# Performance work log

Hardware: AMD Instinct MI355X
Metric: run time of the kernel (lower is better)

The kernel has to match this reference:

```python
import jax, jax.numpy as jnp
import numpy as np

DOT_TEMP = 0.05  # hardcoded in the original forward (self.temperature is never used)
EPS = 1e-6


def setup_inputs() -> dict:
    key = jax.random.key(0)
    k1, k2 = jax.random.split(key)
    bsz, n_views, dim = 4096, 2, 128
    features = jax.random.normal(k1, (bsz, n_views, dim), dtype=jnp.float32)
    labels = jax.random.randint(k2, (bsz,), 0, 100, dtype=jnp.int32)
    return {"features": features, "labels": labels}


def reference(features, labels):
    bsz, V, dim = features.shape  # V = n_views; contrast_mode='all' -> anchor_count = contrast_count = V
    n = V * bsz

    # contrast_feature = cat(unbind(features, dim=1), dim=0): [view0 batch; view1 batch; ...]
    cf = jnp.transpose(features, (1, 0, 2)).reshape(n, dim)  # [n, dim]

    # positive mask: eq(labels, labels.T) tiled, diagonal zeroed
    eq = labels[:, None] == labels[None, :]  # [bsz, bsz]
    mask = jnp.tile(eq.astype(jnp.float32), (V, V))  # [n, n]
    mask = mask * (1.0 - jnp.eye(n, dtype=jnp.float32))

    # Key simplification (exactly faithful): mask3[i] (eq) and mask2[i] (ne) are complementary,
    # so unique(cat(where(mask3[i]), where(mask2[i]))) == arange(n) for every row. Hence each
    # loop iteration in the original computes the SAME scalar from the full gram matrix.
    lab2 = jnp.tile(labels, V)  # matches labels2[:n] layout in the original
    diff = (lab2[:, None] != lab2[None, :]).astype(jnp.float32)  # [n, n]

    dots = jnp.matmul(cf, cf.T) / DOT_TEMP  # [n, n]
    dm = dots * diff
    maxd = jnp.max(dm, axis=1, keepdims=True)
    S = jnp.sum(jnp.exp(dm - maxd))  # exp_terms.sum() -- identical for every valid row
    N = jnp.sum(diff)                # different_label_mask.sum()

    # rows with mask2[i].sum() == 0 are skipped (left at zero)
    valid = jnp.tile(jnp.any(labels[None, :] != labels[:, None], axis=1), V)  # [n]
    xv = jnp.where(valid, S, 0.0)
    nv = jnp.where(valid, N, 0.0)

    # if not all(negtivesum == 0): x = x / negtivesum   (safe divide for skipped rows)
    all_zero = jnp.all(nv == 0.0)
    xv = jnp.where(all_zero, xv, xv / jnp.where(nv == 0.0, 1.0, nv))

    log_prob = -jnp.log(xv[:, None] + EPS)  # [n, 1], broadcast over columns
    msum = jnp.sum(mask, axis=1)
    msum_safe = jnp.where(msum == 0.0, 1.0, msum)
    pos_logits = -jnp.sum(mask * log_prob, axis=1) / msum_safe  # [n]
    loss = jnp.mean(pos_logits)  # mean over view(anchor_count, bsz) == overall mean
    return loss
```

## Files before the change

kernel.cpp:

```cpp
#include <hip/hip_runtime.h>
#include <hip/hip_bf16.h>
#include <stdint.h>

#define N_TOT 8192
#define BSZ   4096
#define NCH   32
#define SQS   5.3715827f

typedef _Float16 f16x8 __attribute__((ext_vector_type(8)));
typedef float f32x4 __attribute__((ext_vector_type(4)));

__device__ __forceinline__ float fast_exp2(float x) {
#if __has_builtin(__builtin_amdgcn_exp2f)
  return __builtin_amdgcn_exp2f(x);
#else
  return exp2f(x);
#endif
}
#define EXP2(x) fast_exp2(x)

__global__ __launch_bounds__(256) void prep14_kernel(
    const float* __restrict__ feat, const int* __restrict__ labels,
    _Float16* __restrict__ H2, unsigned char* __restrict__ lab8, int* __restrict__ cnt) {
  if (blockIdx.x == 512) {
    __shared__ int h[128];
    if (threadIdx.x < 128) h[threadIdx.x] = 0;
    __syncthreads();
    for (int i = threadIdx.x; i < BSZ; i += 256) atomicAdd(&h[labels[i] & 127], 1);
    __syncthreads();
    if (threadIdx.x < 128) cnt[threadIdx.x] = h[threadIdx.x];
    for (int i = threadIdx.x; i < N_TOT; i += 256)
      lab8[i] = (unsigned char)labels[i & (BSZ - 1)];
    return;
  }
  int idx = blockIdx.x * 256 + threadIdx.x;
  int rowblk = idx >> 8, inner = idx & 255;
  int k8 = inner >> 4, rlo = inner & 15;
  int r = rowblk * 16 + rlo;
  int b = r & (BSZ - 1), v = r >> 12;
  const float* src = feat + ((size_t)((b << 1) + v) << 7) + k8 * 8;
  float4 x0 = *(const float4*)src;
  float4 x1 = *(const float4*)(src + 4);
  float xs[8] = {x0.x, x0.y, x0.z, x0.w, x1.x, x1.y, x1.z, x1.w};
  f16x8 hv;
#pragma unroll
  for (int jj = 0; jj < 8; ++jj) hv[jj] = (_Float16)(xs[jj] * SQS);
  *(f16x8*)((char*)H2 + (size_t)idx * 16) = hv;
}

__global__ __launch_bounds__(256) void gemm14_kernel(
    const _Float16* __restrict__ H2, const int* __restrict__ labels,
    const unsigned char* __restrict__ lab8,
    float* __restrict__ pM, float* __restrict__ pS) {
  __shared__ __align__(16) char ldsB[2][16384];

  int orig = blockIdx.x;
  int xcd = orig & 7, j = orig >> 3;
  int cg = xcd * 4 + (j & 3);
  int rg = j >> 2;
  int wave = threadIdx.x >> 6, lane = threadIdx.x & 63;
  int lq = lane >> 4, lr16 = lane & 15;

  const uint32_t rowbase = (uint32_t)rg * 128 + wave * 32;
  const char* Hb = (const char*)H2;
  const uint32_t laneoff = lq * 256 + lr16 * 16;

  int lrw[2];
#pragma unroll
  for (int m = 0; m < 2; ++m)
    lrw[m] = labels[(rowbase + m * 16 + lr16) & (BSZ - 1)];

  f16x8 Areg[2][4];
#pragma unroll
  for (int m = 0; m < 2; ++m)
#pragma unroll
    for (int kb = 0; kb < 4; ++kb)
      Areg[m][kb] = *(const f16x8*)(Hb + (size_t)((rowbase >> 4) + m) * 4096 + kb * 1024 + laneoff);

  const char* Bsrc = Hb + (size_t)cg * 65536;

#define STAGE(T, BUF)                                                                     \
  {                                                                                       \
    _Pragma("unroll")                                                                     \
    for (int i = 0; i < 4; ++i) {                                                         \
      int chunk = wave * 4 + i;                                                           \
      __builtin_amdgcn_global_load_lds(                                                   \
          (const __attribute__((address_space(1))) void*)(Bsrc + ((T) * 4 + (chunk >> 2)) * 4096 + (chunk & 3) * 1024 + lane * 16), \
          (__attribute__((address_space(3))) void*)(&ldsB[BUF][chunk * 1024]), 16, 0, 0); \
    }                                                                                     \
  }

  STAGE(0, 0);
  asm volatile("s_waitcnt vmcnt(0)" ::: "memory");
  __builtin_amdgcn_sched_barrier(0);
  __builtin_amdgcn_s_barrier();

  f32x4 acc[2][4];
  float mxv[2] = {-3.0e38f, -3.0e38f}, sv[2] = {0.0f, 0.0f};

#pragma unroll
  for (int t = 0; t < 4; ++t) {
    if (t < 3) STAGE(t + 1, (t + 1) & 1);
    const char* Bb = ldsB[t & 1];

#pragma unroll
    for (int m = 0; m < 2; ++m)
#pragma unroll
      for (int ni = 0; ni < 4; ++ni) acc[m][ni] = f32x4{0.f, 0.f, 0.f, 0.f};

    f16x8 Bf[2][4];
#pragma unroll
    for (int ni = 0; ni < 4; ++ni)
      Bf[0][ni] = *(const f16x8*)(Bb + ni * 4096 + laneoff);
#pragma unroll
    for (int kb = 0; kb < 4; ++kb) {
      int cur = kb & 1;
      if (kb < 3) {
#pragma unroll
        for (int ni = 0; ni < 4; ++ni)
          Bf[cur ^ 1][ni] = *(const f16x8*)(Bb + ni * 4096 + (kb + 1) * 1024 + laneoff);
      }
      __builtin_amdgcn_s_setprio(1);
#pragma unroll
      for (int m = 0; m < 2; ++m)
#pragma unroll
        for (int ni = 0; ni < 4; ++ni)
          acc[m][ni] = __builtin_amdgcn_mfma_f32_16x16x32_f16(Bf[cur][ni], Areg[m][kb], acc[m][ni], 0, 0, 0);
      __builtin_amdgcn_s_setprio(0);
    }

    uint32_t labw[4];
#pragma unroll
    for (int ni = 0; ni < 4; ++ni)
      labw[ni] = *(const uint32_t*)(lab8 + cg * 256 + t * 64 + ni * 16 + lq * 4);
    int lc[16];
#pragma unroll
    for (int i = 0; i < 16; ++i) lc[i] = (labw[i >> 2] >> (8 * (i & 3))) & 255;

#pragma unroll
    for (int m = 0; m < 2; ++m) {
      float v[16];
#pragma unroll
      for (int ni = 0; ni < 4; ++ni)
#pragma unroll
        for (int r = 0; r < 4; ++r)
          v[ni * 4 + r] = (lrw[m] != lc[ni * 4 + r]) ? acc[m][ni][r] : 0.0f;
      float m01 = fmaxf(v[0], v[1]),  m23 = fmaxf(v[2], v[3]);
      float m45 = fmaxf(v[4], v[5]),  m67 = fmaxf(v[6], v[7]);
      float m89 = fmaxf(v[8], v[9]),  mab = fmaxf(v[10], v[11]);
      float mcd = fmaxf(v[12], v[13]), mef = fmaxf(v[14], v[15]);
      float bm = fmaxf(fmaxf(fmaxf(m01, m23), fmaxf(m45, m67)),
                       fmaxf(fmaxf(m89, mab), fmaxf(mcd, mef)));
      float nm = fmaxf(mxv[m], bm);
      float s0 = 0.f, s1 = 0.f, s2 = 0.f, s3 = 0.f;
#pragma unroll
      for (int r = 0; r < 4; ++r) {
        s0 += EXP2(v[r] - nm);
        s1 += EXP2(v[4 + r] - nm);
        s2 += EXP2(v[8 + r] - nm);
        s3 += EXP2(v[12 + r] - nm);
      }
      sv[m] = sv[m] * EXP2(mxv[m] - nm) + ((s0 + s1) + (s2 + s3));
      mxv[m] = nm;
    }

    asm volatile("s_waitcnt vmcnt(0)" ::: "memory");
    __builtin_amdgcn_sched_barrier(0);
    __builtin_amdgcn_s_barrier();
  }
#undef STAGE

#pragma unroll
  for (int m = 0; m < 2; ++m) {
    float M = mxv[m], S = sv[m];
#pragma unroll
    for (int off = 16; off < 64; off <<= 1) {
      float Mo = __shfl_xor(M, off, 64);
      float So = __shfl_xor(S, off, 64);
      float Mn = fmaxf(M, Mo);
      S = S * EXP2(M - Mn) + So * EXP2(Mo - Mn);
      M = Mn;
    }
    if (lane < 16) {
      pM[(size_t)cg * N_TOT + rowbase + m * 16 + lane] = M;
      pS[(size_t)cg * N_TOT + rowbase + m * 16 + lane] = S;
    }
  }
}

__global__ __launch_bounds__(256) void rowred14_kernel(const float* __restrict__ pM,
                                                       const float* __restrict__ pS,
                                                       float* __restrict__ blockS) {
  int row = blockIdx.x * 256 + threadIdx.x;
  float M = -3.0e38f;
#pragma unroll
  for (int c = 0; c < NCH; ++c) M = fmaxf(M, pM[(size_t)c * N_TOT + row]);
  float s = 0.0f;
#pragma unroll
  for (int c = 0; c < NCH; ++c)
    s += pS[(size_t)c * N_TOT + row] * EXP2(pM[(size_t)c * N_TOT + row] - M);
  __shared__ float red[256];
  red[threadIdx.x] = s;
  __syncthreads();
  for (int st = 128; st > 0; st >>= 1) {
    if (threadIdx.x < st) red[threadIdx.x] += red[threadIdx.x + st];
    __syncthreads();
  }
  if (threadIdx.x == 0) blockS[blockIdx.x] = red[0];
}

__global__ void final14_kernel(const float* __restrict__ blockS, const int* __restrict__ cnt,
                               float* __restrict__ out) {
  int lane = threadIdx.x;
  float s = (lane < 32) ? blockS[lane] : 0.0f;
#pragma unroll
  for (int off = 1; off < 64; off <<= 1) s += __shfl_xor(s, off, 64);
  if (lane == 0) {
    double Stot = (double)s;
    long long sumsq = 0;
    int nval = 0;
    for (int c = 0; c < 128; ++c) {
      long long cc = cnt[c];
      sumsq += cc * cc;
      if (cc > 0 && cc < BSZ) nval += 2 * (int)cc;
    }
    double Nd = (double)N_TOT * (double)N_TOT - 4.0 * (double)sumsq;
    float loss;
    if (Nd <= 0.0 || nval == 0) {
      loss = logf(1e-6f);
    } else {
      float x = (float)(Stot / Nd);
      loss = ((float)nval * logf(x + 1e-6f) +
              (float)(N_TOT - nval) * logf(1e-6f)) / (float)N_TOT;
    }
    out[0] = loss;
  }
}

extern "C" void kernel_launch(void* const* d_in, const int* in_sizes, int n_in,
                              void* d_out, int out_size, void* d_ws, size_t ws_size,
                              hipStream_t stream) {
  const float* feat = (const float*)d_in[0];
  const int* labels = (const int*)d_in[1];
  float* out = (float*)d_out;

  char* ws = (char*)d_ws;
  _Float16* H2        = (_Float16*)(ws);
  unsigned char* lab8 = (unsigned char*)(ws + 2097152);
  float* pM           = (float*)(ws + 2105344);
  float* pS           = (float*)(ws + 3153920);
  int* cnt            = (int*)(ws + 4202496);
  float* blockS       = (float*)(ws + 4203008);

  prep14_kernel<<<513, 256, 0, stream>>>(feat, labels, H2, lab8, cnt);
  gemm14_kernel<<<2048, 256, 0, stream>>>(H2, labels, lab8, pM, pS);
  rowred14_kernel<<<32, 256, 0, stream>>>(pM, pS, blockS);
  final14_kernel<<<1, 64, 0, stream>>>(blockS, cnt, out);
}
```

Before: 46.07 us.

## Fuse final reduction into rowred via atomic counter and trim GEMM registers

Merges the single-block final kernel into the row-reduction kernel. The last block to finish, detected with an atomic counter that the prep kernel resets, computes the loss, which removes one kernel launch. The GEMM kernel gains a launch_bounds occupancy hint of 4 blocks and reads row labels from the byte label array. It also drops the B-fragment double buffering and masks the accumulators in place, cutting register use in exchange for less overlap between LDS loads and MFMA.

```diff
diff --git a/kernel.cpp b/kernel.cpp
--- a/kernel.cpp
+++ b/kernel.cpp
@@ -19,9 +19,10 @@
 }
 #define EXP2(x) fast_exp2(x)
 
-__global__ __launch_bounds__(256) void prep14_kernel(
+__global__ __launch_bounds__(256) void prep16_kernel(
     const float* __restrict__ feat, const int* __restrict__ labels,
-    _Float16* __restrict__ H2, unsigned char* __restrict__ lab8, int* __restrict__ cnt) {
+    _Float16* __restrict__ H2, unsigned char* __restrict__ lab8, int* __restrict__ cnt,
+    int* __restrict__ ctr) {
   if (blockIdx.x == 512) {
     __shared__ int h[128];
     if (threadIdx.x < 128) h[threadIdx.x] = 0;
@@ -29,6 +30,7 @@
     for (int i = threadIdx.x; i < BSZ; i += 256) atomicAdd(&h[labels[i] & 127], 1);
     __syncthreads();
     if (threadIdx.x < 128) cnt[threadIdx.x] = h[threadIdx.x];
+    if (threadIdx.x == 0) *ctr = 0;
     for (int i = threadIdx.x; i < N_TOT; i += 256)
       lab8[i] = (unsigned char)labels[i & (BSZ - 1)];
     return;
@@ -48,9 +50,8 @@
   *(f16x8*)((char*)H2 + (size_t)idx * 16) = hv;
 }
 
-__global__ __launch_bounds__(256) void gemm14_kernel(
-    const _Float16* __restrict__ H2, const int* __restrict__ labels,
-    const unsigned char* __restrict__ lab8,
+__global__ __launch_bounds__(256, 4) void gemm16_kernel(
+    const _Float16* __restrict__ H2, const unsigned char* __restrict__ lab8,
     float* __restrict__ pM, float* __restrict__ pS) {
   __shared__ __align__(16) char ldsB[2][16384];
 
@@ -68,7 +69,7 @@
   int lrw[2];
 #pragma unroll
   for (int m = 0; m < 2; ++m)
-    lrw[m] = labels[(rowbase + m * 16 + lr16) & (BSZ - 1)];
+    lrw[m] = lab8[rowbase + m * 16 + lr16];
 
   f16x8 Areg[2][4];
 #pragma unroll
@@ -108,24 +109,18 @@
 #pragma unroll
       for (int ni = 0; ni < 4; ++ni) acc[m][ni] = f32x4{0.f, 0.f, 0.f, 0.f};
 
-    f16x8 Bf[2][4];
-#pragma unroll
-    for (int ni = 0; ni < 4; ++ni)
-      Bf[0][ni] = *(const f16x8*)(Bb + ni * 4096 + laneoff);
 #pragma unroll
     for (int kb = 0; kb < 4; ++kb) {
-      int cur = kb & 1;
-      if (kb < 3) {
+      f16x8 Bf[4];
+#pragma unroll
+      for (int ni = 0; ni < 4; ++ni)
+        Bf[ni] = *(const f16x8*)(Bb + ni * 4096 + kb * 1024 + laneoff);
+      __builtin_amdgcn_s_setprio(1);
+#pragma unroll
+      for (int m = 0; m < 2; ++m)
 #pragma unroll
         for (int ni = 0; ni < 4; ++ni)
-          Bf[cur ^ 1][ni] = *(const f16x8*)(Bb + ni * 4096 + (kb + 1) * 1024 + laneoff);
-      }
-      __builtin_amdgcn_s_setprio(1);
-#pragma unroll
-      for (int m = 0; m < 2; ++m)
-#pragma unroll
-        for (int ni = 0; ni < 4; ++ni)
-          acc[m][ni] = __builtin_amdgcn_mfma_f32_16x16x32_f16(Bf[cur][ni], Areg[m][kb], acc[m][ni], 0, 0, 0);
+          acc[m][ni] = __builtin_amdgcn_mfma_f32_16x16x32_f16(Bf[ni], Areg[m][kb], acc[m][ni], 0, 0, 0);
       __builtin_amdgcn_s_setprio(0);
     }
 
@@ -133,32 +128,31 @@
 #pragma unroll
     for (int ni = 0; ni < 4; ++ni)
       labw[ni] = *(const uint32_t*)(lab8 + cg * 256 + t * 64 + ni * 16 + lq * 4);
-    int lc[16];
-#pragma unroll
-    for (int i = 0; i < 16; ++i) lc[i] = (labw[i >> 2] >> (8 * (i & 3))) & 255;
+
+#pragma unroll
+    for (int ni = 0; ni < 4; ++ni)
+#pragma unroll
+      for (int r = 0; r < 4; ++r) {
+        int lc = (labw[ni] >> (8 * r)) & 255;
+        acc[0][ni][r] = (lrw[0] != lc) ? acc[0][ni][r] : 0.0f;
+        acc[1][ni][r] = (lrw[1] != lc) ? acc[1][ni][r] : 0.0f;
+      }
 
 #pragma unroll
     for (int m = 0; m < 2; ++m) {
-      float v[16];
-#pragma unroll
-      for (int ni = 0; ni < 4; ++ni)
-#pragma unroll
-        for (int r = 0; r < 4; ++r)
-          v[ni * 4 + r] = (lrw[m] != lc[ni * 4 + r]) ? acc[m][ni][r] : 0.0f;
-      float m01 = fmaxf(v[0], v[1]),  m23 = fmaxf(v[2], v[3]);
-      float m45 = fmaxf(v[4], v[5]),  m67 = fmaxf(v[6], v[7]);
-      float m89 = fmaxf(v[8], v[9]),  mab = fmaxf(v[10], v[11]);
-      float mcd = fmaxf(v[12], v[13]), mef = fmaxf(v[14], v[15]);
-      float bm = fmaxf(fmaxf(fmaxf(m01, m23), fmaxf(m45, m67)),
-                       fmaxf(fmaxf(m89, mab), fmaxf(mcd, mef)));
+      float b0 = fmaxf(fmaxf(acc[m][0][0], acc[m][0][1]), fmaxf(acc[m][0][2], acc[m][0][3]));
+      float b1 = fmaxf(fmaxf(acc[m][1][0], acc[m][1][1]), fmaxf(acc[m][1][2], acc[m][1][3]));
+      float b2 = fmaxf(fmaxf(acc[m][2][0], acc[m][2][1]), fmaxf(acc[m][2][2], acc[m][2][3]));
+      float b3 = fmaxf(fmaxf(acc[m][3][0], acc[m][3][1]), fmaxf(acc[m][3][2], acc[m][3][3]));
+      float bm = fmaxf(fmaxf(b0, b1), fmaxf(b2, b3));
       float nm = fmaxf(mxv[m], bm);
       float s0 = 0.f, s1 = 0.f, s2 = 0.f, s3 = 0.f;
 #pragma unroll
       for (int r = 0; r < 4; ++r) {
-        s0 += EXP2(v[r] - nm);
-        s1 += EXP2(v[4 + r] - nm);
-        s2 += EXP2(v[8 + r] - nm);
-        s3 += EXP2(v[12 + r] - nm);
+        s0 += EXP2(acc[m][0][r] - nm);
+        s1 += EXP2(acc[m][1][r] - nm);
+        s2 += EXP2(acc[m][2][r] - nm);
+        s3 += EXP2(acc[m][3][r] - nm);
       }
       sv[m] = sv[m] * EXP2(mxv[m] - nm) + ((s0 + s1) + (s2 + s3));
       mxv[m] = nm;
@@ -188,9 +182,10 @@
   }
 }
 
-__global__ __launch_bounds__(256) void rowred14_kernel(const float* __restrict__ pM,
-                                                       const float* __restrict__ pS,
-                                                       float* __restrict__ blockS) {
+__global__ __launch_bounds__(256) void rowredfinal16_kernel(
+    const float* __restrict__ pM, const float* __restrict__ pS,
+    const int* __restrict__ cnt, float* __restrict__ blockS,
+    int* __restrict__ ctr, float* __restrict__ out) {
   int row = blockIdx.x * 256 + threadIdx.x;
   float M = -3.0e38f;
 #pragma unroll
@@ -206,34 +201,32 @@
     if (threadIdx.x < st) red[threadIdx.x] += red[threadIdx.x + st];
     __syncthreads();
   }
-  if (threadIdx.x == 0) blockS[blockIdx.x] = red[0];
-}
-
-__global__ void final14_kernel(const float* __restrict__ blockS, const int* __restrict__ cnt,
-                               float* __restrict__ out) {
-  int lane = threadIdx.x;
-  float s = (lane < 32) ? blockS[lane] : 0.0f;
-#pragma unroll
-  for (int off = 1; off < 64; off <<= 1) s += __shfl_xor(s, off, 64);
-  if (lane == 0) {
-    double Stot = (double)s;
-    long long sumsq = 0;
-    int nval = 0;
-    for (int c = 0; c < 128; ++c) {
-      long long cc = cnt[c];
-      sumsq += cc * cc;
-      if (cc > 0 && cc < BSZ) nval += 2 * (int)cc;
-    }
-    double Nd = (double)N_TOT * (double)N_TOT - 4.0 * (double)sumsq;
-    float loss;
-    if (Nd <= 0.0 || nval == 0) {
-      loss = logf(1e-6f);
-    } else {
-      float x = (float)(Stot / Nd);
-      loss = ((float)nval * logf(x + 1e-6f) +
-              (float)(N_TOT - nval) * logf(1e-6f)) / (float)N_TOT;
-    }
-    out[0] = loss;
+  if (threadIdx.x == 0) {
+    blockS[blockIdx.x] = red[0];
+    __threadfence();
+    int old = atomicAdd(ctr, 1);
+    if (old == 31) {
+      __threadfence();
+      double Stot = 0.0;
+      for (int b2 = 0; b2 < 32; ++b2) Stot += (double)blockS[b2];
+      long long sumsq = 0;
+      int nval = 0;
+      for (int c = 0; c < 128; ++c) {
+        long long cc = cnt[c];
+        sumsq += cc * cc;
+        if (cc > 0 && cc < BSZ) nval += 2 * (int)cc;
+      }
+      double Nd = (double)N_TOT * (double)N_TOT - 4.0 * (double)sumsq;
+      float loss;
+      if (Nd <= 0.0 || nval == 0) {
+        loss = logf(1e-6f);
+      } else {
+        float x = (float)(Stot / Nd);
+        loss = ((float)nval * logf(x + 1e-6f) +
+                (float)(N_TOT - nval) * logf(1e-6f)) / (float)N_TOT;
+      }
+      out[0] = loss;
+    }
   }
 }
 
@@ -251,9 +244,9 @@
   float* pS           = (float*)(ws + 3153920);
   int* cnt            = (int*)(ws + 4202496);
   float* blockS       = (float*)(ws + 4203008);
-
-  prep14_kernel<<<513, 256, 0, stream>>>(feat, labels, H2, lab8, cnt);
-  gemm14_kernel<<<2048, 256, 0, stream>>>(H2, labels, lab8, pM, pS);
-  rowred14_kernel<<<32, 256, 0, stream>>>(pM, pS, blockS);
-  final14_kernel<<<1, 64, 0, stream>>>(blockS, cnt, out);
-}
+  int* ctr            = (int*)(ws + 4203136);
+
+  prep16_kernel<<<513, 256, 0, stream>>>(feat, labels, H2, lab8, cnt, ctr);
+  gemm16_kernel<<<2048, 256, 0, stream>>>(H2, lab8, pM, pS);
+  rowredfinal16_kernel<<<32, 256, 0, stream>>>(pM, pS, cnt, blockS, ctr, out);
+}
```

Result: slower. 54.58 us (+18.5%).

## Fuse final reduction into row-reduce kernel and restructure GEMM LDS pipeline waits

Applied to the files above, without the earlier changes.

Merges the last single-block kernel into the row-reduction kernel using an atomic ticket counter, so the last block computes the loss and one launch disappears. The GEMM loop now issues the next tile's global-to-LDS loads before waiting only on the previous tile's loads (vmcnt(4)), which lets the prefetch overlap the current tile's compute and removes one redundant barrier. Row labels are read from the byte label array instead of the int labels. Risks are the correctness of the partial vmcnt wait and the memory ordering of the threadfence and atomic counter.

```diff
diff --git a/kernel.cpp b/kernel.cpp
--- a/kernel.cpp
+++ b/kernel.cpp
@@ -19,9 +19,10 @@
 }
 #define EXP2(x) fast_exp2(x)
 
-__global__ __launch_bounds__(256) void prep14_kernel(
+__global__ __launch_bounds__(256) void prep18_kernel(
     const float* __restrict__ feat, const int* __restrict__ labels,
-    _Float16* __restrict__ H2, unsigned char* __restrict__ lab8, int* __restrict__ cnt) {
+    _Float16* __restrict__ H2, unsigned char* __restrict__ lab8, int* __restrict__ cnt,
+    int* __restrict__ ctr) {
   if (blockIdx.x == 512) {
     __shared__ int h[128];
     if (threadIdx.x < 128) h[threadIdx.x] = 0;
@@ -29,6 +30,7 @@
     for (int i = threadIdx.x; i < BSZ; i += 256) atomicAdd(&h[labels[i] & 127], 1);
     __syncthreads();
     if (threadIdx.x < 128) cnt[threadIdx.x] = h[threadIdx.x];
+    if (threadIdx.x == 0) *ctr = 0;
     for (int i = threadIdx.x; i < N_TOT; i += 256)
       lab8[i] = (unsigned char)labels[i & (BSZ - 1)];
     return;
@@ -48,9 +50,8 @@
   *(f16x8*)((char*)H2 + (size_t)idx * 16) = hv;
 }
 
-__global__ __launch_bounds__(256) void gemm14_kernel(
-    const _Float16* __restrict__ H2, const int* __restrict__ labels,
-    const unsigned char* __restrict__ lab8,
+__global__ __launch_bounds__(256) void gemm18_kernel(
+    const _Float16* __restrict__ H2, const unsigned char* __restrict__ lab8,
     float* __restrict__ pM, float* __restrict__ pS) {
   __shared__ __align__(16) char ldsB[2][16384];
 
@@ -68,7 +69,7 @@
   int lrw[2];
 #pragma unroll
   for (int m = 0; m < 2; ++m)
-    lrw[m] = labels[(rowbase + m * 16 + lr16) & (BSZ - 1)];
+    lrw[m] = lab8[rowbase + m * 16 + lr16];
 
   f16x8 Areg[2][4];
 #pragma unroll
@@ -91,16 +92,20 @@
   }
 
   STAGE(0, 0);
-  asm volatile("s_waitcnt vmcnt(0)" ::: "memory");
-  __builtin_amdgcn_sched_barrier(0);
-  __builtin_amdgcn_s_barrier();
 
   f32x4 acc[2][4];
   float mxv[2] = {-3.0e38f, -3.0e38f}, sv[2] = {0.0f, 0.0f};
 
 #pragma unroll
   for (int t = 0; t < 4; ++t) {
-    if (t < 3) STAGE(t + 1, (t + 1) & 1);
+    if (t < 3) {
+      STAGE(t + 1, (t + 1) & 1);
+      asm volatile("s_waitcnt vmcnt(4)" ::: "memory");
+    } else {
+      asm volatile("s_waitcnt vmcnt(0)" ::: "memory");
+    }
+    __builtin_amdgcn_sched_barrier(0);
+    __builtin_amdgcn_s_barrier();
     const char* Bb = ldsB[t & 1];
 
 #pragma unroll
@@ -164,8 +169,6 @@
       mxv[m] = nm;
     }
 
-    asm volatile("s_waitcnt vmcnt(0)" ::: "memory");
-    __builtin_amdgcn_sched_barrier(0);
     __builtin_amdgcn_s_barrier();
   }
 #undef STAGE
@@ -188,9 +191,10 @@
   }
 }
 
-__global__ __launch_bounds__(256) void rowred14_kernel(const float* __restrict__ pM,
-                                                       const float* __restrict__ pS,
-                                                       float* __restrict__ blockS) {
+__global__ __launch_bounds__(256) void rowredfinal18_kernel(
+    const float* __restrict__ pM, const float* __restrict__ pS,
+    const int* __restrict__ cnt, float* __restrict__ blockS,
+    int* __restrict__ ctr, float* __restrict__ out) {
   int row = blockIdx.x * 256 + threadIdx.x;
   float M = -3.0e38f;
 #pragma unroll
@@ -206,34 +210,32 @@
     if (threadIdx.x < st) red[threadIdx.x] += red[threadIdx.x + st];
     __syncthreads();
   }
-  if (threadIdx.x == 0) blockS[blockIdx.x] = red[0];
-}
-
-__global__ void final14_kernel(const float* __restrict__ blockS, const int* __restrict__ cnt,
-                               float* __restrict__ out) {
-  int lane = threadIdx.x;
-  float s = (lane < 32) ? blockS[lane] : 0.0f;
-#pragma unroll
-  for (int off = 1; off < 64; off <<= 1) s += __shfl_xor(s, off, 64);
-  if (lane == 0) {
-    double Stot = (double)s;
-    long long sumsq = 0;
-    int nval = 0;
-    for (int c = 0; c < 128; ++c) {
-      long long cc = cnt[c];
-      sumsq += cc * cc;
-      if (cc > 0 && cc < BSZ) nval += 2 * (int)cc;
-    }
-    double Nd = (double)N_TOT * (double)N_TOT - 4.0 * (double)sumsq;
-    float loss;
-    if (Nd <= 0.0 || nval == 0) {
-      loss = logf(1e-6f);
-    } else {
-      float x = (float)(Stot / Nd);
-      loss = ((float)nval * logf(x + 1e-6f) +
-              (float)(N_TOT - nval) * logf(1e-6f)) / (float)N_TOT;
-    }
-    out[0] = loss;
+  if (threadIdx.x == 0) {
+    blockS[blockIdx.x] = red[0];
+    __threadfence();
+    int old = atomicAdd(ctr, 1);
+    if (old == 31) {
+      __threadfence();
+      double Stot = 0.0;
+      for (int b2 = 0; b2 < 32; ++b2) Stot += (double)blockS[b2];
+      long long sumsq = 0;
+      int nval = 0;
+      for (int c = 0; c < 128; ++c) {
+        long long cc = cnt[c];
+        sumsq += cc * cc;
+        if (cc > 0 && cc < BSZ) nval += 2 * (int)cc;
+      }
+      double Nd = (double)N_TOT * (double)N_TOT - 4.0 * (double)sumsq;
+      float loss;
+      if (Nd <= 0.0 || nval == 0) {
+        loss = logf(1e-6f);
+      } else {
+        float x = (float)(Stot / Nd);
+        loss = ((float)nval * logf(x + 1e-6f) +
+                (float)(N_TOT - nval) * logf(1e-6f)) / (float)N_TOT;
+      }
+      out[0] = loss;
+    }
   }
 }
 
@@ -251,9 +253,9 @@
   float* pS           = (float*)(ws + 3153920);
   int* cnt            = (int*)(ws + 4202496);
   float* blockS       = (float*)(ws + 4203008);
-
-  prep14_kernel<<<513, 256, 0, stream>>>(feat, labels, H2, lab8, cnt);
-  gemm14_kernel<<<2048, 256, 0, stream>>>(H2, labels, lab8, pM, pS);
-  rowred14_kernel<<<32, 256, 0, stream>>>(pM, pS, blockS);
-  final14_kernel<<<1, 64, 0, stream>>>(blockS, cnt, out);
-}
+  int* ctr            = (int*)(ws + 4203136);
+
+  prep18_kernel<<<513, 256, 0, stream>>>(feat, labels, H2, lab8, cnt, ctr);
+  gemm18_kernel<<<2048, 256, 0, stream>>>(H2, lab8, pM, pS);
+  rowredfinal18_kernel<<<32, 256, 0, stream>>>(pM, pS, cnt, blockS, ctr, out);
+}
```

Result: slower. 47.89 us (+3.9%).
